# Kernel optimization log

Measured on AMD Instinct MI355X. Metric: run time of the kernel, lower is better.

The kernel has to match this reference:

```python
import jax, jax.numpy as jnp
import numpy as np

N_NODES = 100000
N_EDGES = 1600000
D_IN = 64
D_OUT = 64
BN_EPS = 1e-5


def setup_inputs() -> dict:
    key = jax.random.key(0)
    k_x, k_e, k_w, k_b = jax.random.split(key, 4)
    x = jax.random.normal(k_x, (N_NODES, D_IN), dtype=jnp.float32)
    edge_index = jax.random.randint(k_e, (2, N_EDGES), 0, N_NODES, dtype=jnp.int64)
    # GCNConv linear weight (glorot-ish) and bias
    W = jax.random.normal(k_w, (D_IN, D_OUT), dtype=jnp.float32) / np.sqrt(D_IN)
    b = jnp.zeros((D_OUT,), dtype=jnp.float32)
    # BatchNorm affine params (init: weight=1, bias=0)
    bn_weight = jnp.ones((D_OUT,), dtype=jnp.float32)
    bn_bias = jnp.zeros((D_OUT,), dtype=jnp.float32)
    return {"x": x, "edge_index": edge_index, "num_nodes": N_NODES,
            "W": W, "b": b, "bn_weight": bn_weight, "bn_bias": bn_bias}


def reference(x, edge_index, num_nodes, W, b, bn_weight, bn_bias):
    # --- self-loop handling (layer_idx=1) ---
    # _add_custom_self_loops removes existing self-loops and adds 1 per node;
    # PyG gcn_norm's add_remaining_self_loops then keeps exactly one unit-weight
    # self-loop per node. Equivalent (jit-friendly, static shapes): zero-weight
    # any existing self-loop edges and append one self-loop per node.
    src, dst = edge_index[0], edge_index[1]
    ew = (src != dst).astype(x.dtype)                      # [E]
    loop = jnp.arange(num_nodes, dtype=src.dtype)
    src_a = jnp.concatenate([src, loop])                   # [E+N]
    dst_a = jnp.concatenate([dst, loop])
    ew_a = jnp.concatenate([ew, jnp.ones((num_nodes,), x.dtype)])

    # --- symmetric GCN normalization: D^-1/2 A D^-1/2 ---
    deg = jax.ops.segment_sum(ew_a, dst_a, num_segments=num_nodes)  # [N]
    dinv = jnp.where(deg > 0, jax.lax.rsqrt(deg), 0.0)
    norm = dinv[src_a] * ew_a * dinv[dst_a]                # [E+N]

    # --- transform then aggregate (gather -> scatter-add) ---
    h = x @ W                                              # [N, D_OUT]
    msgs = h[src_a] * norm[:, None]                        # [E+N, D_OUT]
    out = jax.ops.segment_sum(msgs, dst_a, num_segments=num_nodes) + b

    # --- BatchNorm (training: batch stats, biased var) + ReLU ---
    mean = jnp.mean(out, axis=0)
    var = jnp.mean(jnp.square(out - mean), axis=0)
    y = (out - mean) * jax.lax.rsqrt(var + BN_EPS) * bn_weight + bn_bias
    return jax.nn.relu(y)
```

## Files before the change

### kernel.cpp

```cpp
#include <hip/hip_runtime.h>

#define NN 100000
#define D 64
#define BN_EPS 1e-5f

typedef unsigned short ushort_t;
typedef unsigned int uint_t;

__device__ __forceinline__ ushort_t f2b_rne(float f) {
    uint_t u = __float_as_uint(f);
    uint_t r = (u + 0x7FFFu + ((u >> 16) & 1u)) >> 16;
    return (ushort_t)r;
}
__device__ __forceinline__ float b2f(ushort_t u) {
    return __uint_as_float(((uint_t)u) << 16);
}


__global__ void k_zero(int* cnt, float* sums8, int n) {
    int i = blockIdx.x * blockDim.x + threadIdx.x;
    if (i < n) cnt[i] = 0;
    if (i < 1152) sums8[i] = 0.0f;
}

__global__ void k_count4(const int* __restrict__ src, const int* __restrict__ dst,
                         int* cnt, int E) {
    int t = blockIdx.x * blockDim.x + threadIdx.x;
    int e0 = t * 4;
    if (e0 >= E) return;
    if (e0 + 4 <= E) {
        int4 s4 = *(const int4*)(src + e0);
        int4 d4 = *(const int4*)(dst + e0);
        if (s4.x != d4.x) atomicAdd(&cnt[d4.x], 1);
        if (s4.y != d4.y) atomicAdd(&cnt[d4.y], 1);
        if (s4.z != d4.z) atomicAdd(&cnt[d4.z], 1);
        if (s4.w != d4.w) atomicAdd(&cnt[d4.w], 1);
    } else {
        for (int e = e0; e < E; ++e) {
            int s = src[e], d = dst[e];
            if (s != d) atomicAdd(&cnt[d], 1);
        }
    }
}

__global__ void k_dinv_i(const int* __restrict__ cnt, float* dinv, int n) {
    int i = blockIdx.x * blockDim.x + threadIdx.x;
    if (i < n) dinv[i] = rsqrtf((float)cnt[i] + 1.0f);
}

__global__ void k_xb(const float* __restrict__ x, const float* __restrict__ dinv,
                     ushort_t* __restrict__ xb, int n) {
    int i = blockIdx.x * blockDim.x + threadIdx.x;
    int total = n * (D / 4);
    if (i >= total) return;
    int row = i >> 4;
    float di = dinv[row];
    float4 v = ((const float4*)x)[i];
    ushort4 o;
    o.x = f2b_rne(v.x * di);
    o.y = f2b_rne(v.y * di);
    o.z = f2b_rne(v.z * di);
    o.w = f2b_rne(v.w * di);
    ((ushort4*)xb)[i] = o;
}

__global__ __launch_bounds__(1024) void k_scanA(const int* __restrict__ cnt,
                                                int* __restrict__ row_ptr,
                                                int* __restrict__ bsum, int n) {
    __shared__ int sm[1024];
    int tid = threadIdx.x;
    int i = blockIdx.x * 1024 + tid;
    int v = (i < n) ? cnt[i] : 0;
    int xv = v;
    sm[tid] = xv;
    __syncthreads();
    for (int off = 1; off < 1024; off <<= 1) {
        int t = (tid >= off) ? sm[tid - off] : 0;
        __syncthreads();
        xv += t;
        sm[tid] = xv;
        __syncthreads();
    }
    if (i < n) row_ptr[i] = xv - v;
    if (tid == 1023) bsum[blockIdx.x] = xv;
}

__global__ void k_scanB(int* bsum, int nb) {
    __shared__ int sm[128];
    int tid = threadIdx.x;
    int v = (tid < nb) ? bsum[tid] : 0;
    int xv = v;
    sm[tid] = xv;
    __syncthreads();
    for (int off = 1; off < 128; off <<= 1) {
        int t = (tid >= off) ? sm[tid - off] : 0;
        __syncthreads();
        xv += t;
        sm[tid] = xv;
        __syncthreads();
    }
    if (tid < nb) bsum[tid] = xv - v;
}

__global__ void k_scanC(int* __restrict__ row_ptr, int* __restrict__ cursor,
                        const int* __restrict__ bsum, int n) {
    int i = blockIdx.x * blockDim.x + threadIdx.x;
    if (i < n) {
        int r = row_ptr[i] + bsum[i >> 10];
        row_ptr[i] = r;
        cursor[i] = r;
    }
}

__global__ void k_place8(const int* __restrict__ src, const int* __restrict__ dst,
                         int* cursor, int* __restrict__ srcid, int E) {
    int t = blockIdx.x * blockDim.x + threadIdx.x;
    int e0 = t * 8;
    if (e0 >= E) return;
    if (e0 + 8 <= E) {
        int4 sa = *(const int4*)(src + e0);
        int4 sb = *(const int4*)(src + e0 + 4);
        int4 da = *(const int4*)(dst + e0);
        int4 db = *(const int4*)(dst + e0 + 4);
        if (sa.x != da.x) srcid[atomicAdd(&cursor[da.x], 1)] = sa.x;
        if (sa.y != da.y) srcid[atomicAdd(&cursor[da.y], 1)] = sa.y;
        if (sa.z != da.z) srcid[atomicAdd(&cursor[da.z], 1)] = sa.z;
        if (sa.w != da.w) srcid[atomicAdd(&cursor[da.w], 1)] = sa.w;
        if (sb.x != db.x) srcid[atomicAdd(&cursor[db.x], 1)] = sb.x;
        if (sb.y != db.y) srcid[atomicAdd(&cursor[db.y], 1)] = sb.y;
        if (sb.z != db.z) srcid[atomicAdd(&cursor[db.z], 1)] = sb.z;
        if (sb.w != db.w) srcid[atomicAdd(&cursor[db.w], 1)] = sb.w;
    } else {
        for (int e = e0; e < E; ++e) {
            int s = src[e], d = dst[e];
            if (s != d) srcid[atomicAdd(&cursor[d], 1)] = s;
        }
    }
}

__global__ __launch_bounds__(256) void k_gather_gemm_stats_bf16(
        const int* __restrict__ row_ptr, const int* __restrict__ cnt,
        const int* __restrict__ srcid, const float* __restrict__ x,
        const ushort_t* __restrict__ xb, const float* __restrict__ dinv,
        const float* __restrict__ W, float* __restrict__ out, float* sums8, int n) {
    __shared__ float Ws[64 * 64];
    int tid = threadIdx.x;
    for (int i = tid; i < 64 * 64; i += 256) Ws[i] = W[i];
    __syncthreads();
    int wave = tid >> 6, lane = tid & 63;
    float s = 0.0f, sq = 0.0f;
    for (int d = blockIdx.x * 4 + wave; d < n; d += gridDim.x * 4) {
        int base = row_ptr[d];
        int c = cnt[d];
        float did = dinv[d];
        float self = x[(size_t)d * D + lane];
        float acc = 0.0f;
        int j = 0;
        for (; j + 8 <= c; j += 8) {
            int si[8];
            float xv[8];
#pragma unroll
            for (int u = 0; u < 8; ++u) si[u] = srcid[base + j + u];
#pragma unroll
            for (int u = 0; u < 8; ++u) xv[u] = b2f(xb[(size_t)si[u] * D + lane]);
#pragma unroll
            for (int u = 0; u < 8; ++u) acc += xv[u];
        }
        for (; j < c; ++j) {
            int si = srcid[base + j];
            acc += b2f(xb[(size_t)si * D + lane]);
        }
        float agg = did * (did * self + acc);
        float o = 0.0f;
#pragma unroll
        for (int k = 0; k < 64; ++k) {
            o += __shfl(agg, k) * Ws[k * 64 + lane];
        }
        out[(size_t)d * D + lane] = o;
        s += o;
        sq += o * o;
    }
    __shared__ float ls[4][64], lq[4][64];
    ls[wave][lane] = s;
    lq[wave][lane] = sq;
    __syncthreads();
    if (wave == 0) {
        float ts = ls[0][lane] + ls[1][lane] + ls[2][lane] + ls[3][lane];
        float tq = lq[0][lane] + lq[1][lane] + lq[2][lane] + lq[3][lane];
        float* slot = sums8 + (size_t)(blockIdx.x & 7) * 128;
        atomicAdd(&slot[lane], ts);
        atomicAdd(&slot[64 + lane], tq);
    }
}

__global__ __launch_bounds__(256) void k_gather_gemm_stats(
        const int* __restrict__ row_ptr, const int* __restrict__ cnt,
        const int* __restrict__ srcid, const float* __restrict__ x,
        const float* __restrict__ dinv, const float* __restrict__ W,
        float* __restrict__ out, float* sums8, int n) {
    __shared__ float Ws[64 * 64];
    int tid = threadIdx.x;
    for (int i = tid; i < 64 * 64; i += 256) Ws[i] = W[i];
    __syncthreads();
    int wave = tid >> 6, lane = tid & 63;
    float s = 0.0f, sq = 0.0f;
    for (int d = blockIdx.x * 4 + wave; d < n; d += gridDim.x * 4) {
        int base = row_ptr[d];
        int c = cnt[d];
        float did = dinv[d];
        float acc = x[(size_t)d * D + lane] * did * did;
        int j = 0;
        for (; j + 8 <= c; j += 8) {
            int si[8];
            float wv[8], xv[8];
#pragma unroll
            for (int u = 0; u < 8; ++u) si[u] = srcid[base + j + u];
#pragma unroll
            for (int u = 0; u < 8; ++u) wv[u] = dinv[si[u]] * did;
#pragma unroll
            for (int u = 0; u < 8; ++u) xv[u] = x[(size_t)si[u] * D + lane];
#pragma unroll
            for (int u = 0; u < 8; ++u) acc += xv[u] * wv[u];
        }
        for (; j < c; ++j) {
            int si = srcid[base + j];
            acc += x[(size_t)si * D + lane] * (dinv[si] * did);
        }
        float o = 0.0f;
#pragma unroll
        for (int k = 0; k < 64; ++k) {
            o += __shfl(acc, k) * Ws[k * 64 + lane];
        }
        out[(size_t)d * D + lane] = o;
        s += o;
        sq += o * o;
    }
    __shared__ float ls[4][64], lq[4][64];
    ls[wave][lane] = s;
    lq[wave][lane] = sq;
    __syncthreads();
    if (wave == 0) {
        float ts = ls[0][lane] + ls[1][lane] + ls[2][lane] + ls[3][lane];
        float tq = lq[0][lane] + lq[1][lane] + lq[2][lane] + lq[3][lane];
        float* slot = sums8 + (size_t)(blockIdx.x & 7) * 128;
        atomicAdd(&slot[lane], ts);
        atomicAdd(&slot[64 + lane], tq);
    }
}

__global__ void k_finalize(float* sums8) {
    int i = threadIdx.x;
    float s = 0.0f;
#pragma unroll
    for (int j = 0; j < 8; ++j) s += sums8[j * 128 + i];
    sums8[1024 + i] = s;
}

__global__ void k_bn_apply(float* out, const float* __restrict__ sums,
                           const float* __restrict__ bnw, const float* __restrict__ bnb,
                           int n) {
    int i = blockIdx.x * blockDim.x + threadIdx.x;
    int total = n * (D / 4);
    if (i >= total) return;
    int c0 = (i * 4) & 63;
    const float invn = 1.0f / (float)NN;
    float4 v = ((const float4*)out)[i];
    float r[4] = {v.x, v.y, v.z, v.w};
#pragma unroll
    for (int j = 0; j < 4; ++j) {
        int c = c0 + j;
        float mean = sums[c] * invn;
        float var = sums[64 + c] * invn - mean * mean;
        if (var < 0.0f) var = 0.0f;
        float scale = bnw[c] * rsqrtf(var + BN_EPS);
        float y = (r[j] - mean) * scale + bnb[c];
        r[j] = y > 0.0f ? y : 0.0f;
    }
    float4 o = {r[0], r[1], r[2], r[3]};
    ((float4*)out)[i] = o;
}

extern "C" void kernel_launch(void* const* d_in, const int* in_sizes, int n_in,
                              void* d_out, int out_size, void* d_ws, size_t ws_size,
                              hipStream_t stream) {
    const float* x = (const float*)d_in[0];
    const int* ei = (const int*)d_in[1];
    const float* W = (const float*)d_in[3];
    const float* bnw = (const float*)d_in[5];
    const float* bnb = (const float*)d_in[6];
    float* out = (float*)d_out;

    const int n = in_sizes[0] / D;
    const int E = in_sizes[1] / 2;
    const int* src = ei;
    const int* dst = ei + E;

    const size_t base_words = (size_t)4 * n + (size_t)E + 1280;
    const size_t need_csr = base_words * 4;
    const size_t need_bf16 = need_csr + 16 + (size_t)n * D * 2;

    if (ws_size >= need_csr) {
        int* cnt = (int*)d_ws;
        int* row_ptr = cnt + n;
        int* cursor = row_ptr + n;
        float* dinv = (float*)(cursor + n);
        int* srcid = (int*)(dinv + n);
        int* bsum = srcid + E;
        float* sums8 = (float*)(bsum + 128);
        float* sums = sums8 + 1024;
        size_t off = ((size_t)(sums8 + 1152 - (float*)d_ws) * 4 + 15) & ~(size_t)15;
        ushort_t* xb = (ushort_t*)((char*)d_ws + off);

        const int nb = (n + 1023) / 1024;

        k_zero<<<(n + 255) / 256, 256, 0, stream>>>(cnt, sums8, n);
        k_count4<<<((E + 3) / 4 + 255) / 256, 256, 0, stream>>>(src, dst, cnt, E);
        k_dinv_i<<<(n + 255) / 256, 256, 0, stream>>>(cnt, dinv, n);
        k_scanA<<<nb, 1024, 0, stream>>>(cnt, row_ptr, bsum, n);
        k_scanB<<<1, 128, 0, stream>>>(bsum, nb);
        k_scanC<<<(n + 255) / 256, 256, 0, stream>>>(row_ptr, cursor, bsum, n);
        k_place8<<<((E + 7) / 8 + 255) / 256, 256, 0, stream>>>(src, dst, cursor, srcid, E);

        if (ws_size >= need_bf16) {
            k_xb<<<(n * (D / 4) + 255) / 256, 256, 0, stream>>>(x, dinv, xb, n);
            k_gather_gemm_stats_bf16<<<4096, 256, 0, stream>>>(row_ptr, cnt, srcid, x, xb,
                                                               dinv, W, out, sums8, n);
        } else {
            k_gather_gemm_stats<<<4096, 256, 0, stream>>>(row_ptr, cnt, srcid, x, dinv, W,
                                                          out, sums8, n);
        }
        k_finalize<<<1, 128, 0, stream>>>(sums8);
        k_bn_apply<<<(n * (D / 4) + 255) / 256, 256, 0, stream>>>(out, sums, bnw, bnb, n);
    }
}
```

Baseline: 399.2 us.

## Gather two nodes per wave with packed bf16 pairs and fuse dinv with bf16 cast

The gather/GEMM kernel now handles two destination nodes per wave, each half-wave lane loading a packed pair of bf16 features, and the 64x64 transform uses double-packed shuffles. It launches one block per 8 nodes instead of a grid-stride loop. The dinv computation is fused into the bf16 conversion kernel, edge counting processes 8 edges per thread, and the BN partial-sum slots grow from 8 to 16 to spread atomic contention. The fp32 fallback and workspace-size checks are removed, which assumes a large enough workspace.

```diff
diff --git a/kernel.cpp b/kernel.cpp
--- a/kernel.cpp
+++ b/kernel.cpp
@@ -12,29 +12,34 @@
     uint_t r = (u + 0x7FFFu + ((u >> 16) & 1u)) >> 16;
     return (ushort_t)r;
 }
-__device__ __forceinline__ float b2f(ushort_t u) {
-    return __uint_as_float(((uint_t)u) << 16);
-}
-
-
-__global__ void k_zero(int* cnt, float* sums8, int n) {
+__device__ __forceinline__ float b2f_lo(uint_t u) { return __uint_as_float(u << 16); }
+__device__ __forceinline__ float b2f_hi(uint_t u) { return __uint_as_float(u & 0xFFFF0000u); }
+
+
+__global__ void k_zero(int* cnt, float* sums16, int n) {
     int i = blockIdx.x * blockDim.x + threadIdx.x;
     if (i < n) cnt[i] = 0;
-    if (i < 1152) sums8[i] = 0.0f;
-}
-
-__global__ void k_count4(const int* __restrict__ src, const int* __restrict__ dst,
+    if (i < 2176) sums16[i] = 0.0f;
+}
+
+__global__ void k_count8(const int* __restrict__ src, const int* __restrict__ dst,
                          int* cnt, int E) {
     int t = blockIdx.x * blockDim.x + threadIdx.x;
-    int e0 = t * 4;
+    int e0 = t * 8;
     if (e0 >= E) return;
-    if (e0 + 4 <= E) {
-        int4 s4 = *(const int4*)(src + e0);
-        int4 d4 = *(const int4*)(dst + e0);
-        if (s4.x != d4.x) atomicAdd(&cnt[d4.x], 1);
-        if (s4.y != d4.y) atomicAdd(&cnt[d4.y], 1);
-        if (s4.z != d4.z) atomicAdd(&cnt[d4.z], 1);
-        if (s4.w != d4.w) atomicAdd(&cnt[d4.w], 1);
+    if (e0 + 8 <= E) {
+        int4 sa = *(const int4*)(src + e0);
+        int4 sb = *(const int4*)(src + e0 + 4);
+        int4 da = *(const int4*)(dst + e0);
+        int4 db = *(const int4*)(dst + e0 + 4);
+        if (sa.x != da.x) atomicAdd(&cnt[da.x], 1);
+        if (sa.y != da.y) atomicAdd(&cnt[da.y], 1);
+        if (sa.z != da.z) atomicAdd(&cnt[da.z], 1);
+        if (sa.w != da.w) atomicAdd(&cnt[da.w], 1);
+        if (sb.x != db.x) atomicAdd(&cnt[db.x], 1);
+        if (sb.y != db.y) atomicAdd(&cnt[db.y], 1);
+        if (sb.z != db.z) atomicAdd(&cnt[db.z], 1);
+        if (sb.w != db.w) atomicAdd(&cnt[db.w], 1);
     } else {
         for (int e = e0; e < E; ++e) {
             int s = src[e], d = dst[e];
@@ -43,18 +48,14 @@
     }
 }
 
-__global__ void k_dinv_i(const int* __restrict__ cnt, float* dinv, int n) {
-    int i = blockIdx.x * blockDim.x + threadIdx.x;
-    if (i < n) dinv[i] = rsqrtf((float)cnt[i] + 1.0f);
-}
-
-__global__ void k_xb(const float* __restrict__ x, const float* __restrict__ dinv,
-                     ushort_t* __restrict__ xb, int n) {
+__global__ void k_dinv_xb(const int* __restrict__ cnt, const float* __restrict__ x,
+                          float* __restrict__ dinv, ushort_t* __restrict__ xb, int n) {
     int i = blockIdx.x * blockDim.x + threadIdx.x;
     int total = n * (D / 4);
     if (i >= total) return;
     int row = i >> 4;
-    float di = dinv[row];
+    float di = rsqrtf((float)cnt[row] + 1.0f);
+    if ((i & 15) == 0) dinv[row] = di;
     float4 v = ((const float4*)x)[i];
     ushort4 o;
     o.x = f2b_rne(v.x * di);
@@ -138,122 +139,103 @@
     }
 }
 
-__global__ __launch_bounds__(256) void k_gather_gemm_stats_bf16(
+__global__ __launch_bounds__(256) void k_gather2(
         const int* __restrict__ row_ptr, const int* __restrict__ cnt,
         const int* __restrict__ srcid, const float* __restrict__ x,
         const ushort_t* __restrict__ xb, const float* __restrict__ dinv,
-        const float* __restrict__ W, float* __restrict__ out, float* sums8, int n) {
+        const float* __restrict__ W, float* __restrict__ out, float* sums16, int n) {
     __shared__ float Ws[64 * 64];
     int tid = threadIdx.x;
     for (int i = tid; i < 64 * 64; i += 256) Ws[i] = W[i];
     __syncthreads();
+
     int wave = tid >> 6, lane = tid & 63;
-    float s = 0.0f, sq = 0.0f;
-    for (int d = blockIdx.x * 4 + wave; d < n; d += gridDim.x * 4) {
-        int base = row_ptr[d];
-        int c = cnt[d];
-        float did = dinv[d];
-        float self = x[(size_t)d * D + lane];
-        float acc = 0.0f;
-        int j = 0;
-        for (; j + 8 <= c; j += 8) {
-            int si[8];
-            float xv[8];
-#pragma unroll
-            for (int u = 0; u < 8; ++u) si[u] = srcid[base + j + u];
-#pragma unroll
-            for (int u = 0; u < 8; ++u) xv[u] = b2f(xb[(size_t)si[u] * D + lane]);
-#pragma unroll
-            for (int u = 0; u < 8; ++u) acc += xv[u];
-        }
-        for (; j < c; ++j) {
-            int si = srcid[base + j];
-            acc += b2f(xb[(size_t)si * D + lane]);
-        }
-        float agg = did * (did * self + acc);
-        float o = 0.0f;
-#pragma unroll
-        for (int k = 0; k < 64; ++k) {
-            o += __shfl(agg, k) * Ws[k * 64 + lane];
-        }
-        out[(size_t)d * D + lane] = o;
-        s += o;
-        sq += o * o;
-    }
-    __shared__ float ls[4][64], lq[4][64];
-    ls[wave][lane] = s;
-    lq[wave][lane] = sq;
+    int sl = lane & 31;
+    int half = lane >> 5;
+    int c0 = sl * 2;
+    int d = blockIdx.x * 8 + wave * 2 + half;
+    bool valid = d < n;
+
+    int base = 0, c = 0;
+    float did = 0.0f;
+    float2 self = {0.0f, 0.0f};
+    if (valid) {
+        base = row_ptr[d];
+        c = cnt[d];
+        did = dinv[d];
+        self = *(const float2*)&x[(size_t)d * D + c0];
+    }
+
+    float2 acc = {0.0f, 0.0f};
+    for (int j = 0; j < c; j += 8) {
+        int si[8];
+        uint_t rv[8];
+#pragma unroll
+        for (int u = 0; u < 8; ++u) {
+            int idx = j + u;
+            si[u] = srcid[base + (idx < c ? idx : c - 1)];
+        }
+#pragma unroll
+        for (int u = 0; u < 8; ++u) {
+            rv[u] = *(const uint_t*)&xb[(size_t)si[u] * D + c0];
+        }
+#pragma unroll
+        for (int u = 0; u < 8; ++u) {
+            if (j + u < c) {
+                acc.x += b2f_lo(rv[u]);
+                acc.y += b2f_hi(rv[u]);
+            }
+        }
+    }
+
+    float2 agg;
+    agg.x = did * (did * self.x + acc.x);
+    agg.y = did * (did * self.y + acc.y);
+
+    double pk = __hiloint2double(__float_as_int(agg.y), __float_as_int(agg.x));
+    float2 o = {0.0f, 0.0f};
+    int hb = lane & 32;
+#pragma unroll
+    for (int m = 0; m < 32; ++m) {
+        double t = __shfl(pk, hb + m);
+        float ax = __uint_as_float((uint_t)__double2loint(t));
+        float ay = __uint_as_float((uint_t)__double2hiint(t));
+        float2 w0 = *(const float2*)&Ws[(2 * m) * 64 + c0];
+        float2 w1 = *(const float2*)&Ws[(2 * m + 1) * 64 + c0];
+        o.x += ax * w0.x + ay * w1.x;
+        o.y += ax * w0.y + ay * w1.y;
+    }
+    if (valid) *(float2*)&out[(size_t)d * D + c0] = o;
+
+    float2 s2 = valid ? o : make_float2(0.0f, 0.0f);
+    float2 q2 = {s2.x * s2.x, s2.y * s2.y};
+    __shared__ float2 ls[4][64], lq[4][64];
+    ls[wave][lane] = s2;
+    lq[wave][lane] = q2;
     __syncthreads();
-    if (wave == 0) {
-        float ts = ls[0][lane] + ls[1][lane] + ls[2][lane] + ls[3][lane];
-        float tq = lq[0][lane] + lq[1][lane] + lq[2][lane] + lq[3][lane];
-        float* slot = sums8 + (size_t)(blockIdx.x & 7) * 128;
-        atomicAdd(&slot[lane], ts);
-        atomicAdd(&slot[64 + lane], tq);
-    }
-}
-
-__global__ __launch_bounds__(256) void k_gather_gemm_stats(
-        const int* __restrict__ row_ptr, const int* __restrict__ cnt,
-        const int* __restrict__ srcid, const float* __restrict__ x,
-        const float* __restrict__ dinv, const float* __restrict__ W,
-        float* __restrict__ out, float* sums8, int n) {
-    __shared__ float Ws[64 * 64];
-    int tid = threadIdx.x;
-    for (int i = tid; i < 64 * 64; i += 256) Ws[i] = W[i];
-    __syncthreads();
-    int wave = tid >> 6, lane = tid & 63;
-    float s = 0.0f, sq = 0.0f;
-    for (int d = blockIdx.x * 4 + wave; d < n; d += gridDim.x * 4) {
-        int base = row_ptr[d];
-        int c = cnt[d];
-        float did = dinv[d];
-        float acc = x[(size_t)d * D + lane] * did * did;
-        int j = 0;
-        for (; j + 8 <= c; j += 8) {
-            int si[8];
-            float wv[8], xv[8];
-#pragma unroll
-            for (int u = 0; u < 8; ++u) si[u] = srcid[base + j + u];
-#pragma unroll
-            for (int u = 0; u < 8; ++u) wv[u] = dinv[si[u]] * did;
-#pragma unroll
-            for (int u = 0; u < 8; ++u) xv[u] = x[(size_t)si[u] * D + lane];
-#pragma unroll
-            for (int u = 0; u < 8; ++u) acc += xv[u] * wv[u];
-        }
-        for (; j < c; ++j) {
-            int si = srcid[base + j];
-            acc += x[(size_t)si * D + lane] * (dinv[si] * did);
-        }
-        float o = 0.0f;
-#pragma unroll
-        for (int k = 0; k < 64; ++k) {
-            o += __shfl(acc, k) * Ws[k * 64 + lane];
-        }
-        out[(size_t)d * D + lane] = o;
-        s += o;
-        sq += o * o;
-    }
-    __shared__ float ls[4][64], lq[4][64];
-    ls[wave][lane] = s;
-    lq[wave][lane] = sq;
-    __syncthreads();
-    if (wave == 0) {
-        float ts = ls[0][lane] + ls[1][lane] + ls[2][lane] + ls[3][lane];
-        float tq = lq[0][lane] + lq[1][lane] + lq[2][lane] + lq[3][lane];
-        float* slot = sums8 + (size_t)(blockIdx.x & 7) * 128;
-        atomicAdd(&slot[lane], ts);
-        atomicAdd(&slot[64 + lane], tq);
-    }
-}
-
-__global__ void k_finalize(float* sums8) {
+    if (wave == 0 && lane < 32) {
+        float2 ts = {0.0f, 0.0f}, tq = {0.0f, 0.0f};
+#pragma unroll
+        for (int w = 0; w < 4; ++w) {
+            ts.x += ls[w][lane].x + ls[w][lane + 32].x;
+            ts.y += ls[w][lane].y + ls[w][lane + 32].y;
+            tq.x += lq[w][lane].x + lq[w][lane + 32].x;
+            tq.y += lq[w][lane].y + lq[w][lane + 32].y;
+        }
+        float* slot = sums16 + (size_t)(blockIdx.x & 15) * 128;
+        atomicAdd(&slot[c0], ts.x);
+        atomicAdd(&slot[c0 + 1], ts.y);
+        atomicAdd(&slot[64 + c0], tq.x);
+        atomicAdd(&slot[64 + c0 + 1], tq.y);
+    }
+}
+
+__global__ void k_finalize(float* sums16) {
     int i = threadIdx.x;
     float s = 0.0f;
 #pragma unroll
-    for (int j = 0; j < 8; ++j) s += sums8[j * 128 + i];
-    sums8[1024 + i] = s;
+    for (int j = 0; j < 16; ++j) s += sums16[j * 128 + i];
+    sums16[2048 + i] = s;
 }
 
 __global__ void k_bn_apply(float* out, const float* __restrict__ sums,
@@ -295,41 +277,29 @@
     const int* src = ei;
     const int* dst = ei + E;
 
-    const size_t base_words = (size_t)4 * n + (size_t)E + 1280;
-    const size_t need_csr = base_words * 4;
-    const size_t need_bf16 = need_csr + 16 + (size_t)n * D * 2;
-
-    if (ws_size >= need_csr) {
-        int* cnt = (int*)d_ws;
-        int* row_ptr = cnt + n;
-        int* cursor = row_ptr + n;
-        float* dinv = (float*)(cursor + n);
-        int* srcid = (int*)(dinv + n);
-        int* bsum = srcid + E;
-        float* sums8 = (float*)(bsum + 128);
-        float* sums = sums8 + 1024;
-        size_t off = ((size_t)(sums8 + 1152 - (float*)d_ws) * 4 + 15) & ~(size_t)15;
-        ushort_t* xb = (ushort_t*)((char*)d_ws + off);
-
-        const int nb = (n + 1023) / 1024;
-
-        k_zero<<<(n + 255) / 256, 256, 0, stream>>>(cnt, sums8, n);
-        k_count4<<<((E + 3) / 4 + 255) / 256, 256, 0, stream>>>(src, dst, cnt, E);
-        k_dinv_i<<<(n + 255) / 256, 256, 0, stream>>>(cnt, dinv, n);
-        k_scanA<<<nb, 1024, 0, stream>>>(cnt, row_ptr, bsum, n);
-        k_scanB<<<1, 128, 0, stream>>>(bsum, nb);
-        k_scanC<<<(n + 255) / 256, 256, 0, stream>>>(row_ptr, cursor, bsum, n);
-        k_place8<<<((E + 7) / 8 + 255) / 256, 256, 0, stream>>>(src, dst, cursor, srcid, E);
-
-        if (ws_size >= need_bf16) {
-            k_xb<<<(n * (D / 4) + 255) / 256, 256, 0, stream>>>(x, dinv, xb, n);
-            k_gather_gemm_stats_bf16<<<4096, 256, 0, stream>>>(row_ptr, cnt, srcid, x, xb,
-                                                               dinv, W, out, sums8, n);
-        } else {
-            k_gather_gemm_stats<<<4096, 256, 0, stream>>>(row_ptr, cnt, srcid, x, dinv, W,
-                                                          out, sums8, n);
-        }
-        k_finalize<<<1, 128, 0, stream>>>(sums8);
-        k_bn_apply<<<(n * (D / 4) + 255) / 256, 256, 0, stream>>>(out, sums, bnw, bnb, n);
-    }
-}
+    int* cnt = (int*)d_ws;
+    int* row_ptr = cnt + n;
+    int* cursor = row_ptr + n;
+    float* dinv = (float*)(cursor + n);
+    int* srcid = (int*)(dinv + n);
+    int* bsum = srcid + E;
+    float* sums16 = (float*)(bsum + 128);
+    float* sums = sums16 + 2048;
+    size_t off = ((size_t)((char*)(sums16 + 2176) - (char*)d_ws) + 15) & ~(size_t)15;
+    ushort_t* xb = (ushort_t*)((char*)d_ws + off);
+
+    const int nb = (n + 1023) / 1024;
+
+    k_zero<<<(n + 255) / 256, 256, 0, stream>>>(cnt, sums16, n);
+    k_count8<<<((E + 7) / 8 + 255) / 256, 256, 0, stream>>>(src, dst, cnt, E);
+    k_dinv_xb<<<(n * (D / 4) + 255) / 256, 256, 0, stream>>>(cnt, x, dinv, xb, n);
+    k_scanA<<<nb, 1024, 0, stream>>>(cnt, row_ptr, bsum, n);
+    k_scanB<<<1, 128, 0, stream>>>(bsum, nb);
+    k_scanC<<<(n + 255) / 256, 256, 0, stream>>>(row_ptr, cursor, bsum, n);
+    k_place8<<<((E + 7) / 8 + 255) / 256, 256, 0, stream>>>(src, dst, cursor, srcid, E);
+
+    k_gather2<<<(n + 7) / 8, 256, 0, stream>>>(row_ptr, cnt, srcid, x, xb, dinv, W,
+                                               out, sums16, n);
+    k_finalize<<<1, 128, 0, stream>>>(sums16);
+    k_bn_apply<<<(n * (D / 4) + 255) / 256, 256, 0, stream>>>(out, sums, bnw, bnb, n);
+}
```

New measurement: 373.0 us. 6.6% less time.
